# Performance work log

Hardware: AMD Instinct MI355X
Metric: run time of the kernel (lower is better)

The kernel has to match this reference:

```python
import jax, jax.numpy as jnp
import numpy as np

B, C, H, W = 32, 512, 64, 64
K = 512  # num_embeddings == embedding_dim == C (required by the original view())
COMMIT = 0.25


def setup_inputs() -> dict:
    key = jax.random.key(0)
    k1, k2 = jax.random.split(key)
    x = jax.random.normal(k1, (B, C, H, W), dtype=jnp.float32)
    # nn.Embedding weight init: uniform(-1/K, 1/K)
    embed = jax.random.uniform(k2, (K, C), dtype=jnp.float32, minval=-1.0 / K, maxval=1.0 / K)
    return {"x": x, "embed": embed}


def reference(x, embed):
    # BCHW -> BHWC
    inputs = jnp.transpose(x, (0, 2, 3, 1))  # [B,H,W,C]
    flat = inputs.reshape(-1, C)              # [N,C], N = B*H*W
    d = (jnp.sum(flat * flat, axis=1, keepdims=True)
         + jnp.sum(embed * embed, axis=1)
         - 2.0 * flat @ embed.T)              # [N,K]
    idx = jnp.argmin(d, axis=1)               # [N]
    # one-hot @ embed  ==  gather
    quantized = embed[idx].reshape(inputs.shape)  # [B,H,W,C]

    e_latent = jnp.mean((jax.lax.stop_gradient(quantized) - inputs) ** 2)
    q_latent = jnp.mean((quantized - jax.lax.stop_gradient(inputs)) ** 2)
    loss = q_latent + COMMIT * e_latent

    # straight-through estimator
    quant_st = inputs + jax.lax.stop_gradient(quantized - inputs)

    # perplexity (as in source: mean over batch of #unique codes used)
    idx_b = idx.reshape(B, -1)                # [B, H*W]

    def n_unique(i):
        cnt = jnp.zeros((K,), jnp.int32).at[i].add(1)
        return jnp.sum(cnt > 0)

    perplexity = jnp.mean(jax.vmap(n_unique)(idx_b).astype(jnp.float32))

    return loss, jnp.transpose(quant_st, (0, 3, 1, 2)), perplexity, idx_b
```

## Files before the change

kernel.cpp:

```cpp
#include <hip/hip_runtime.h>
#include <stdint.h>

#define B_ 32
#define C_ 512
#define HW_ 4096
#define N_ 131072
#define K_ 512
#define QELEMS 67108864
#define MARGIN 1e-3f
#define CAND   2.5e-3f
#define MAXC   16
#define RFCAP 131072

typedef __attribute__((ext_vector_type(8)))  short bf16x8;
typedef __attribute__((ext_vector_type(16))) float f32x16;

__device__ __forceinline__ ushort f2bf(float f) {
  uint u = __float_as_uint(f);
  return (ushort)((u + 0x7FFFu + ((u >> 16) & 1u)) >> 16);
}

__device__ __forceinline__ float np_pw512(const float* a) {
  float P[4];
#pragma unroll
  for (int m = 0; m < 4; ++m) {
    const float* q = a + m * 128;
    float rv[16];
#pragma unroll
    for (int l = 0; l < 16; ++l) {
      float v0 = q[l],      v1 = q[16 + l],  v2 = q[32 + l],  v3 = q[48 + l];
      float v4 = q[64 + l], v5 = q[80 + l],  v6 = q[96 + l],  v7 = q[112 + l];
      rv[l] = ((v0 + v1) + (v2 + v3)) + ((v4 + v5) + (v6 + v7));
    }
    float u[8], w[4];
#pragma unroll
    for (int l = 0; l < 8; ++l) u[l] = rv[8 + l] + rv[l];
#pragma unroll
    for (int l = 0; l < 4; ++l) w[l] = u[4 + l] + u[l];
    P[m] = (w[0] + w[2]) + (w[1] + w[3]);
  }
  return (P[0] + P[1]) + (P[2] + P[3]);
}

__device__ __forceinline__ float np_pw512_sq(const float* a) {
  float P[4];
#pragma unroll
  for (int m = 0; m < 4; ++m) {
    const float* q = a + m * 128;
    float rv[16];
#pragma unroll
    for (int l = 0; l < 16; ++l) {
      float v0 = __fmul_rn(q[l], q[l]);
      float v1 = __fmul_rn(q[16 + l], q[16 + l]);
      float v2 = __fmul_rn(q[32 + l], q[32 + l]);
      float v3 = __fmul_rn(q[48 + l], q[48 + l]);
      float v4 = __fmul_rn(q[64 + l], q[64 + l]);
      float v5 = __fmul_rn(q[80 + l], q[80 + l]);
      float v6 = __fmul_rn(q[96 + l], q[96 + l]);
      float v7 = __fmul_rn(q[112 + l], q[112 + l]);
      rv[l] = ((v0 + v1) + (v2 + v3)) + ((v4 + v5) + (v6 + v7));
    }
    float u[8], w[4];
#pragma unroll
    for (int l = 0; l < 8; ++l) u[l] = rv[8 + l] + rv[l];
#pragma unroll
    for (int l = 0; l < 4; ++l) w[l] = u[4 + l] + u[l];
    P[m] = (w[0] + w[2]) + (w[1] + w[3]);
  }
  return (P[0] + P[1]) + (P[2] + P[3]);
}

__global__ __launch_bounds__(256) void k_prep(const float* __restrict__ embed,
    float* __restrict__ senp, float* __restrict__ eT, int* __restrict__ rcnt,
    int* __restrict__ ocnt, int* __restrict__ candCnt)
{
  __shared__ float sqa[C_];
  int k = blockIdx.x;
  candCnt[blockIdx.x * 256 + threadIdx.x] = 0;
  for (int c = threadIdx.x; c < C_; c += 256) {
    float e = embed[k * C_ + c];
    eT[c * K_ + k] = e;
    sqa[c] = __fmul_rn(e, e);
  }
  __syncthreads();
  if (threadIdx.x == 0) {
    senp[k] = np_pw512(sqa);
    if (blockIdx.x == 0) { *rcnt = 0; *ocnt = 0; }
  }
}

__global__ __launch_bounds__(256) void k_epack(const float* __restrict__ embed,
    ushort* __restrict__ efrag)
{
  const int cb = blockIdx.x;
  const int t = threadIdx.x;
  const int lane = t & 63, ksq = t >> 6;
  const int l31 = lane & 31, lhi = lane >> 5;
  const float* ep = embed + ((size_t)(cb * 32 + l31) << 9) + lhi * 8;
#pragma unroll
  for (int i = 0; i < 8; ++i) {
    int ks = ksq * 8 + i;
    float4 v0 = *(const float4*)(ep + ks * 16);
    float4 v1 = *(const float4*)(ep + ks * 16 + 4);
    uint u0 = (uint)f2bf(v0.x) | ((uint)f2bf(v0.y) << 16);
    uint u1 = (uint)f2bf(v0.z) | ((uint)f2bf(v0.w) << 16);
    uint u2 = (uint)f2bf(v1.x) | ((uint)f2bf(v1.y) << 16);
    uint u3 = (uint)f2bf(v1.z) | ((uint)f2bf(v1.w) << 16);
    ushort* op = efrag + (((size_t)(cb * 32 + ks)) * 64 + lane) * 8;
    *(uint4*)op = make_uint4(u0, u1, u2, u3);
  }
}

__global__ __launch_bounds__(256) void k_xsplit(const float* __restrict__ x,
    ushort* __restrict__ xfrag, float* __restrict__ xT)
{
  __shared__ float tile[64][66];
  const int bid = blockIdx.x;
  const int ht = bid & 63, ct = (bid >> 6) & 7, b = bid >> 9;
  const int t = threadIdx.x;
  const int r = t & 63, cq = t >> 6;
  const float* xp = x + (((size_t)(b * C_ + ct * 64)) << 12) + ht * 64 + r;
#pragma unroll
  for (int i = 0; i < 16; ++i) {
    int c = cq * 16 + i;
    tile[r][c] = xp[(size_t)c << 12];
  }
  __syncthreads();
  const int lane = t & 63, ksl = t >> 6;
  const int l31 = lane & 31, lhi = lane >> 5;
  const int ks = ct * 4 + ksl;
  const int cc = ksl * 16 + lhi * 8;
#pragma unroll
  for (int rbl = 0; rbl < 2; ++rbl) {
    int rr = rbl * 32 + l31;
    uint u[4];
#pragma unroll
    for (int j = 0; j < 4; ++j) {
      float f0 = tile[rr][cc + 2 * j];
      float f1 = tile[rr][cc + 2 * j + 1];
      u[j] = (uint)f2bf(f0) | ((uint)f2bf(f1) << 16);
    }
    size_t rb = (size_t)b * 128 + ht * 2 + rbl;
    ushort* op = xfrag + ((rb * 32 + ks) * 64 + lane) * 8;
    *(uint4*)op = make_uint4(u[0], u[1], u[2], u[3]);
  }
  if (xT) {
    const int r2 = t >> 2, cs2 = (t & 3) << 4;
    float* op = xT + ((size_t)(b * HW_ + ht * 64 + r2) << 9) + ct * 64 + cs2;
#pragma unroll
    for (int j = 0; j < 4; ++j) {
      float4 v;
      v.x = tile[r2][cs2 + 4 * j + 0];
      v.y = tile[r2][cs2 + 4 * j + 1];
      v.z = tile[r2][cs2 + 4 * j + 2];
      v.w = tile[r2][cs2 + 4 * j + 3];
      *(float4*)(op + 4 * j) = v;
    }
  }
}

__global__ __launch_bounds__(512, 2) void k_argmin(const ushort* __restrict__ xfrag,
    const ushort* __restrict__ efrag, const float* __restrict__ senp,
    int* __restrict__ idx_out, int* __restrict__ rcnt, int* __restrict__ rrows,
    int* __restrict__ candCnt, int* __restrict__ cand)
{
  __shared__ float ses[K_];
  __shared__ float mbL[128][4], msL[128][4];
  __shared__ int   miL[128][4];
  __shared__ float rowBest[128];
  __shared__ int   rowFlag[128];
  const int t = threadIdx.x;
  const int lane = t & 63, wid = t >> 6;
  const int wc = wid & 3, wr = wid >> 2;
  const int l31 = lane & 31, lhi = lane >> 5;
  const int bid = blockIdx.x;

  for (int i = t; i < K_; i += 512) ses[i] = senp[i];
  __syncthreads();

  const size_t rb0 = (size_t)bid * 4 + wr * 2;
  const bf16x8* xq0 = (const bf16x8*)xfrag + rb0 * 2048 + lane;
  const bf16x8* xq1 = xq0 + 2048;
  const bf16x8* eq0 = (const bf16x8*)efrag + (size_t)(wc * 4 + 0) * 2048 + lane;
  const bf16x8* eq1 = eq0 + 2048;
  const bf16x8* eq2 = eq0 + 4096;
  const bf16x8* eq3 = eq0 + 6144;

  f32x16 z = {0,0,0,0,0,0,0,0,0,0,0,0,0,0,0,0};
  f32x16 a00 = z, a01 = z, a02 = z, a03 = z;
  f32x16 a10 = z, a11 = z, a12 = z, a13 = z;
  __builtin_amdgcn_s_setprio(1);
#pragma unroll 8
  for (int ks = 0; ks < 32; ++ks) {
    bf16x8 x0 = xq0[ks * 64];
    bf16x8 x1 = xq1[ks * 64];
    bf16x8 e0 = eq0[ks * 64];
    bf16x8 e1 = eq1[ks * 64];
    bf16x8 e2 = eq2[ks * 64];
    bf16x8 e3 = eq3[ks * 64];
    a00 = __builtin_amdgcn_mfma_f32_32x32x16_bf16(e0, x0, a00, 0, 0, 0);
    a01 = __builtin_amdgcn_mfma_f32_32x32x16_bf16(e1, x0, a01, 0, 0, 0);
    a02 = __builtin_amdgcn_mfma_f32_32x32x16_bf16(e2, x0, a02, 0, 0, 0);
    a03 = __builtin_amdgcn_mfma_f32_32x32x16_bf16(e3, x0, a03, 0, 0, 0);
    a10 = __builtin_amdgcn_mfma_f32_32x32x16_bf16(e0, x1, a10, 0, 0, 0);
    a11 = __builtin_amdgcn_mfma_f32_32x32x16_bf16(e1, x1, a11, 0, 0, 0);
    a12 = __builtin_amdgcn_mfma_f32_32x32x16_bf16(e2, x1, a12, 0, 0, 0);
    a13 = __builtin_amdgcn_mfma_f32_32x32x16_bf16(e3, x1, a13, 0, 0, 0);
  }
  __builtin_amdgcn_s_setprio(0);

  float b0 = 1e30f, s0 = 1e30f; int i0 = 0;
#pragma unroll
  for (int r = 0; r < 16; ++r) {
    int crow = (r & 3) + 8 * (r >> 2) + 4 * lhi;
    float v; int code;
    code = wc * 128 + 0  + crow; v = ses[code] - 2.0f * a00[r];
    if (v < b0 || (v == b0 && code < i0)) { s0 = b0; b0 = v; i0 = code; }
    else if (v < s0) s0 = v;
    code = wc * 128 + 32 + crow; v = ses[code] - 2.0f * a01[r];
    if (v < b0 || (v == b0 && code < i0)) { s0 = b0; b0 = v; i0 = code; }
    else if (v < s0) s0 = v;
    code = wc * 128 + 64 + crow; v = ses[code] - 2.0f * a02[r];
    if (v < b0 || (v == b0 && code < i0)) { s0 = b0; b0 = v; i0 = code; }
    else if (v < s0) s0 = v;
    code = wc * 128 + 96 + crow; v = ses[code] - 2.0f * a03[r];
    if (v < b0 || (v == b0 && code < i0)) { s0 = b0; b0 = v; i0 = code; }
    else if (v < s0) s0 = v;
  }
  float b1 = 1e30f, s1 = 1e30f; int i1 = 0;
#pragma unroll
  for (int r = 0; r < 16; ++r) {
    int crow = (r & 3) + 8 * (r >> 2) + 4 * lhi;
    float v; int code;
    code = wc * 128 + 0  + crow; v = ses[code] - 2.0f * a10[r];
    if (v < b1 || (v == b1 && code < i1)) { s1 = b1; b1 = v; i1 = code; }
    else if (v < s1) s1 = v;
    code = wc * 128 + 32 + crow; v = ses[code] - 2.0f * a11[r];
    if (v < b1 || (v == b1 && code < i1)) { s1 = b1; b1 = v; i1 = code; }
    else if (v < s1) s1 = v;
    code = wc * 128 + 64 + crow; v = ses[code] - 2.0f * a12[r];
    if (v < b1 || (v == b1 && code < i1)) { s1 = b1; b1 = v; i1 = code; }
    else if (v < s1) s1 = v;
    code = wc * 128 + 96 + crow; v = ses[code] - 2.0f * a13[r];
    if (v < b1 || (v == b1 && code < i1)) { s1 = b1; b1 = v; i1 = code; }
    else if (v < s1) s1 = v;
  }
  const float pb0 = b0, ps0 = s0; const int pi0 = i0;
  const float pb1 = b1, ps1 = s1; const int pi1 = i1;
  {
    float ob = __shfl_xor(b0, 32, 64), os = __shfl_xor(s0, 32, 64);
    int   oi = __shfl_xor(i0, 32, 64);
    float ns = fminf(fmaxf(b0, ob), fminf(s0, os));
    if (ob < b0 || (ob == b0 && oi < i0)) { b0 = ob; i0 = oi; }
    s0 = ns;
  }
  {
    float ob = __shfl_xor(b1, 32, 64), os = __shfl_xor(s1, 32, 64);
    int   oi = __shfl_xor(i1, 32, 64);
    float ns = fminf(fmaxf(b1, ob), fminf(s1, os));
    if (ob < b1 || (ob == b1 && oi < i1)) { b1 = ob; i1 = oi; }
    s1 = ns;
  }
  if (lane < 32) {
    int rr0 = (wr * 2 + 0) * 32 + l31;
    int rr1 = (wr * 2 + 1) * 32 + l31;
    mbL[rr0][wc] = b0; msL[rr0][wc] = s0; miL[rr0][wc] = i0;
    mbL[rr1][wc] = b1; msL[rr1][wc] = s1; miL[rr1][wc] = i1;
  }
  __syncthreads();
  if (t < 128) {
    float Bv = 1e30f, Sv = 1e30f; int Iv = 0;
#pragma unroll
    for (int q = 0; q < 4; ++q) {
      float bq = mbL[t][q], sq = msL[t][q]; int iq = miL[t][q];
      if (bq < Bv || (bq == Bv && iq < Iv)) { Sv = fminf(Bv, sq); Bv = bq; Iv = iq; }
      else Sv = fminf(Sv, bq);
    }
    int n = bid * 128 + t;
    idx_out[n] = Iv;
    rowBest[t] = Bv;
    int fl = (Sv - Bv < MARGIN) ? 1 : 0;
    rowFlag[t] = fl;
    if (fl) {
      int p = atomicAdd(rcnt, 1);
      if (p < RFCAP) rrows[p] = n;
    }
  }
  __syncthreads();
  {
    const int rr0 = (wr * 2 + 0) * 32 + l31;
    if (rowFlag[rr0]) {
      const float thr = rowBest[rr0] + CAND;
      const int n = bid * 128 + rr0;
      if (pb0 <= thr) {
        int p = atomicAdd(&candCnt[n], 1);
        if (p < MAXC) cand[(size_t)n * MAXC + p] = pi0;
      }
      if (ps0 <= thr) {
#pragma unroll
        for (int r = 0; r < 16; ++r) {
          int crow = (r & 3) + 8 * (r >> 2) + 4 * lhi;
          float v; int code;
          code = wc * 128 + 0  + crow; v = ses[code] - 2.0f * a00[r];
          if (v <= thr && code != pi0) { int p = atomicAdd(&candCnt[n], 1); if (p < MAXC) cand[(size_t)n * MAXC + p] = code; }
          code = wc * 128 + 32 + crow; v = ses[code] - 2.0f * a01[r];
          if (v <= thr && code != pi0) { int p = atomicAdd(&candCnt[n], 1); if (p < MAXC) cand[(size_t)n * MAXC + p] = code; }
          code = wc * 128 + 64 + crow; v = ses[code] - 2.0f * a02[r];
          if (v <= thr && code != pi0) { int p = atomicAdd(&candCnt[n], 1); if (p < MAXC) cand[(size_t)n * MAXC + p] = code; }
          code = wc * 128 + 96 + crow; v = ses[code] - 2.0f * a03[r];
          if (v <= thr && code != pi0) { int p = atomicAdd(&candCnt[n], 1); if (p < MAXC) cand[(size_t)n * MAXC + p] = code; }
        }
      }
    }
    const int rr1 = (wr * 2 + 1) * 32 + l31;
    if (rowFlag[rr1]) {
      const float thr = rowBest[rr1] + CAND;
      const int n = bid * 128 + rr1;
      if (pb1 <= thr) {
        int p = atomicAdd(&candCnt[n], 1);
        if (p < MAXC) cand[(size_t)n * MAXC + p] = pi1;
      }
      if (ps1 <= thr) {
#pragma unroll
        for (int r = 0; r < 16; ++r) {
          int crow = (r & 3) + 8 * (r >> 2) + 4 * lhi;
          float v; int code;
          code = wc * 128 + 0  + crow; v = ses[code] - 2.0f * a10[r];
          if (v <= thr && code != pi1) { int p = atomicAdd(&candCnt[n], 1); if (p < MAXC) cand[(size_t)n * MAXC + p] = code; }
          code = wc * 128 + 32 + crow; v = ses[code] - 2.0f * a11[r];
          if (v <= thr && code != pi1) { int p = atomicAdd(&candCnt[n], 1); if (p < MAXC) cand[(size_t)n * MAXC + p] = code; }
          code = wc * 128 + 64 + crow; v = ses[code] - 2.0f * a12[r];
          if (v <= thr && code != pi1) { int p = atomicAdd(&candCnt[n], 1); if (p < MAXC) cand[(size_t)n * MAXC + p] = code; }
          code = wc * 128 + 96 + crow; v = ses[code] - 2.0f * a13[r];
          if (v <= thr && code != pi1) { int p = atomicAdd(&candCnt[n], 1); if (p < MAXC) cand[(size_t)n * MAXC + p] = code; }
        }
      }
    }
  }
}

__global__ __launch_bounds__(256) void k_refine(const float* __restrict__ x,
    const float* __restrict__ xT, const float* __restrict__ embed,
    const float* __restrict__ senp,
    const int* __restrict__ rcnt, const int* __restrict__ rrows,
    const int* __restrict__ candCnt, const int* __restrict__ cand,
    int* __restrict__ ocnt, int* __restrict__ olist,
    int* __restrict__ idx_out)
{
  __shared__ float xls[4][516];
  __shared__ float SxSh[4];
  __shared__ int   nrow[4];
  const int t = threadIdx.x;
  const int lane = t & 63, w = t >> 6;
  int cnt = *rcnt; if (cnt > RFCAP) cnt = RFCAP;
  for (int base = blockIdx.x * 4; base < cnt; base += gridDim.x * 4) {
    __syncthreads();
    if (t < 4) {
      int i = base + t;
      nrow[t] = rrows[i < cnt ? i : base];
    }
    __syncthreads();
    if (xT) {
      for (int i = t; i < 4 * C_; i += 256) {
        int s = i >> 9, c = i & 511;
        xls[s][c] = xT[((size_t)nrow[s] << 9) + c];
      }
    } else {
      for (int i = t; i < 4 * C_; i += 256) {
        int s = i >> 9, c = i & 511;
        int n = nrow[s];
        int b = n >> 12, hw = n & 4095;
        xls[s][c] = x[(((size_t)(b * C_ + c)) << 12) + hw];
      }
    }
    __syncthreads();
    if (t < 4) SxSh[t] = np_pw512_sq(&xls[t][0]);
    __syncthreads();
    const int n = nrow[w];
    const int cc = candCnt[n];
    float d = 1e30f; int code = 0x7fffffff;
    if (cc <= MAXC) {
      if (lane < cc) {
        code = cand[(size_t)n * MAXC + lane];
        const float* e = embed + (size_t)code * C_;
        const float* xr = &xls[w][0];
        float s1 = 0.f, s2 = 0.f;
        for (int c = 0; c < 384; ++c)  s1 = fmaf(xr[c], e[c], s1);
        for (int c = 384; c < 512; ++c) s2 = fmaf(xr[c], e[c], s2);
        float M = s1 + s2;
        d = (SxSh[w] + senp[code]) - 2.0f * M;
      }
#pragma unroll
      for (int off = 1; off < 16; off <<= 1) {
        float ov = __shfl_xor(d, off, 64);
        int   oc = __shfl_xor(code, off, 64);
        if (ov < d || (ov == d && oc < code)) { d = ov; code = oc; }
      }
      if (lane == 0 && base + w < cnt) idx_out[n] = code;
    } else {
      if (lane == 0 && base + w < cnt) {
        int p = atomicAdd(ocnt, 1);
        if (p < RFCAP) olist[p] = n;
      }
    }
  }
}

__global__ __launch_bounds__(512) void k_refine_full(const float* __restrict__ x,
    const float* __restrict__ xT, const float* __restrict__ eT,
    const float* __restrict__ senp,
    const int* __restrict__ rcnt, const int* __restrict__ rrows,
    int* __restrict__ idx_out)
{
  __shared__ float xls[8][520];
  __shared__ float SxSh[8];
  __shared__ int   nrow[8];
  __shared__ float wval[8][8];
  __shared__ int   widx[8][8];
  const int t = threadIdx.x;
  const int lane = t & 63, w = t >> 6;
  int cnt = *rcnt; if (cnt > RFCAP) cnt = RFCAP;
  for (int base = blockIdx.x * 8; base < cnt; base += gridDim.x * 8) {
    __syncthreads();
    if (t < 8) {
      int i = base + t;
      nrow[t] = rrows[i < cnt ? i : base];
    }
    __syncthreads();
    if (xT) {
#pragma unroll
      for (int rr = 0; rr < 8; ++rr)
        xls[rr][t] = xT[((size_t)nrow[rr] << 9) + t];
    } else {
#pragma unroll
      for (int rr = 0; rr < 8; ++rr) {
        int n = nrow[rr];
        int b = n >> 12, hw = n & 4095;
        xls[rr][t] = x[(((size_t)(b * C_ + t)) << 12) + hw];
      }
    }
    __syncthreads();
    if (t < 8) SxSh[t] = np_pw512_sq(&xls[t][0]);
    __syncthreads();
    const float* ep = eT + t;
    float a1[8], a2[8];
#pragma unroll
    for (int rr = 0; rr < 8; ++rr) { a1[rr] = 0.f; a2[rr] = 0.f; }
    for (int c4 = 0; c4 < 384; c4 += 4) {
      float e0 = ep[(size_t)(c4 + 0) << 9];
      float e1 = ep[(size_t)(c4 + 1) << 9];
      float e2 = ep[(size_t)(c4 + 2) << 9];
      float e3 = ep[(size_t)(c4 + 3) << 9];
#pragma unroll
      for (int rr = 0; rr < 8; ++rr) {
        float4 xv = *(const float4*)&xls[rr][c4];
        a1[rr] = fmaf(xv.x, e0, a1[rr]);
        a1[rr] = fmaf(xv.y, e1, a1[rr]);
        a1[rr] = fmaf(xv.z, e2, a1[rr]);
        a1[rr] = fmaf(xv.w, e3, a1[rr]);
      }
    }
    for (int c4 = 384; c4 < 512; c4 += 4) {
      float e0 = ep[(size_t)(c4 + 0) << 9];
      float e1 = ep[(size_t)(c4 + 1) << 9];
      float e2 = ep[(size_t)(c4 + 2) << 9];
      float e3 = ep[(size_t)(c4 + 3) << 9];
#pragma unroll
      for (int rr = 0; rr < 8; ++rr) {
        float4 xv = *(const float4*)&xls[rr][c4];
        a2[rr] = fmaf(xv.x, e0, a2[rr]);
        a2[rr] = fmaf(xv.y, e1, a2[rr]);
        a2[rr] = fmaf(xv.z, e2, a2[rr]);
        a2[rr] = fmaf(xv.w, e3, a2[rr]);
      }
    }
    float se = senp[t];
    float bv[8]; int bi[8];
#pragma unroll
    for (int rr = 0; rr < 8; ++rr) {
      float M = a1[rr] + a2[rr];
      bv[rr] = (SxSh[rr] + se) - 2.0f * M;
      bi[rr] = t;
    }
#pragma unroll
    for (int off = 1; off < 64; off <<= 1) {
#pragma unroll
      for (int rr = 0; rr < 8; ++rr) {
        float ov = __shfl_xor(bv[rr], off, 64);
        int   oi = __shfl_xor(bi[rr], off, 64);
        if (ov < bv[rr] || (ov == bv[rr] && oi < bi[rr])) { bv[rr] = ov; bi[rr] = oi; }
      }
    }
    if (lane == 0) {
#pragma unroll
      for (int rr = 0; rr < 8; ++rr) { wval[w][rr] = bv[rr]; widx[w][rr] = bi[rr]; }
    }
    __syncthreads();
    if (t < 8) {
      float Bv = wval[0][t]; int Iv = widx[0][t];
#pragma unroll
      for (int q = 1; q < 8; ++q) {
        float ov = wval[q][t]; int oi = widx[q][t];
        if (ov < Bv || (ov == Bv && oi < Iv)) { Bv = ov; Iv = oi; }
      }
      if (base + t < cnt) idx_out[nrow[t]] = Iv;
    }
  }
}

__global__ __launch_bounds__(256) void k_gather(const float* __restrict__ x,
    const float* __restrict__ embed, const int* __restrict__ idx,
    float* __restrict__ out_q, double* __restrict__ loss_part)
{
  __shared__ float ecol[32][512];
  const int bid = blockIdx.x;
  const int hch = bid & 1, cch = (bid >> 1) & 15, b = bid >> 5;
  const int c0 = cch * 32, hw0 = hch * 2048;
  const int t = threadIdx.x;
  for (int i = t; i < 512 * 32; i += 256) {
    int c = i & 31, k = i >> 5;
    ecol[c][(k + c0 + c) & 511] = embed[((size_t)k << 9) + c0 + c];
  }
  __syncthreads();
  int kreg[8];
#pragma unroll
  for (int j = 0; j < 8; ++j)
    kreg[j] = idx[(b << 12) + hw0 + t + 256 * j];
  double s = 0.0;
  for (int c = 0; c < 32; ++c) {
    const float* xrow = x + (((size_t)(b * C_ + c0 + c)) << 12) + hw0;
    float* orow = out_q + (((size_t)(b * C_ + c0 + c)) << 12) + hw0;
#pragma unroll
    for (int j = 0; j < 8; ++j) {
      float q  = ecol[c][(kreg[j] + c0 + c) & 511];
      float xv = xrow[t + 256 * j];
      orow[t + 256 * j] = q;
      double d = (double)q - (double)xv;
      s += d * d;
    }
  }
  for (int off = 32; off > 0; off >>= 1) s += __shfl_down(s, off, 64);
  __shared__ double wsum[4];
  if ((t & 63) == 0) wsum[t >> 6] = s;
  __syncthreads();
  if (t == 0)
    loss_part[bid] = (wsum[0] + wsum[1]) + (wsum[2] + wsum[3]);
}

__global__ __launch_bounds__(256) void k_pplx(const int* __restrict__ idx,
    float* __restrict__ out_idxf, int* __restrict__ counts)
{
  __shared__ int flags[K_];
  __shared__ int red[256];
  int b = blockIdx.x;
  for (int i = threadIdx.x; i < K_; i += 256) flags[i] = 0;
  __syncthreads();
  for (int hw = threadIdx.x; hw < HW_; hw += 256) {
    int k = idx[(b << 12) + hw];
    flags[k] = 1;
    out_idxf[(b << 12) + hw] = (float)k;
  }
  __syncthreads();
  int c = 0;
  for (int i = threadIdx.x; i < K_; i += 256) c += flags[i];
  red[threadIdx.x] = c;
  __syncthreads();
  for (int st = 128; st > 0; st >>= 1) {
    if (threadIdx.x < st) red[threadIdx.x] += red[threadIdx.x + st];
    __syncthreads();
  }
  if (threadIdx.x == 0) counts[b] = red[0];
}

__global__ __launch_bounds__(256) void k_final(const double* __restrict__ loss_part,
    const int* __restrict__ counts, float* __restrict__ out_loss,
    float* __restrict__ out_pplx)
{
  __shared__ double sred[256];
  double s = 0.0;
  for (int i = threadIdx.x; i < 1024; i += 256) s += loss_part[i];
  sred[threadIdx.x] = s;
  __syncthreads();
  for (int st = 128; st > 0; st >>= 1) {
    if (threadIdx.x < st) sred[threadIdx.x] += sred[threadIdx.x + st];
    __syncthreads();
  }
  if (threadIdx.x == 0) {
    *out_loss = (float)(1.25 * sred[0] / (double)QELEMS);
    int c = 0;
    for (int i = 0; i < B_; ++i) c += counts[i];
    *out_pplx = (float)c / (float)B_;
  }
}

extern "C" void kernel_launch(void* const* d_in, const int* in_sizes, int n_in,
                              void* d_out, int out_size, void* d_ws, size_t ws_size,
                              hipStream_t stream)
{
  const float* x     = (const float*)d_in[0];
  const float* embed = (const float*)d_in[1];
  float* out      = (float*)d_out;
  float* out_loss = out;
  float* out_q    = out + 1;
  float* out_pplx = out + 1 + QELEMS;
  float* out_idxf = out + 2 + QELEMS;

  char* ws = (char*)d_ws;
  int*    w_idx = (int*)ws;
  double* w_lp  = (double*)(ws + 524288);
  int*    w_cnt = (int*)(ws + 524288 + 16384);
  size_t pers = 524288 + 16384 + 128;

  const size_t SZ_XFR  = 134217728;
  const size_t SZ_EFR  = 524288;
  const size_t SZ_SENP = 2048;
  const size_t SZ_RCNT = 256;
  const size_t SZ_RROW = (size_t)RFCAP * 4;
  const size_t SZ_OLST = (size_t)RFCAP * 4;
  const size_t SZ_ET   = (size_t)K_ * C_ * 4;
  const size_t SZ_CCNT = (size_t)N_ * 4;
  const size_t SZ_CAND = (size_t)N_ * MAXC * 4;
  const size_t SZ_XT   = (size_t)N_ * C_ * 4;
  const size_t VOL_SMALL = SZ_XFR + SZ_EFR + SZ_SENP + SZ_RCNT + SZ_RROW +
                           SZ_OLST + SZ_ET + SZ_CCNT + SZ_CAND;
  const size_t VOL_BIG   = VOL_SMALL + SZ_XT;

  char* vbase;
  float* w_xT = nullptr;
  if (ws_size >= pers + VOL_BIG + 4096) {
    vbase = ws + ((pers + 255) & ~(size_t)255);
    w_xT  = (float*)(vbase + VOL_SMALL);
  } else if (ws_size >= pers + VOL_SMALL + 4096) {
    vbase = ws + ((pers + 255) & ~(size_t)255);
  } else {
    uintptr_t a = ((uintptr_t)(out_q + QELEMS) - VOL_SMALL) & ~(uintptr_t)255;
    vbase = (char*)a;
  }
  char* p = vbase;
  ushort* w_xfr  = (ushort*)p;            p += SZ_XFR;
  ushort* w_efr  = (ushort*)p;            p += SZ_EFR;
  float*  w_senp = (float*)p;             p += SZ_SENP;
  int*    w_rcnt = (int*)p;
  int*    w_ocnt = (int*)(p + 128);       p += SZ_RCNT;
  int*    w_rrows= (int*)p;               p += SZ_RROW;
  int*    w_olst = (int*)p;               p += SZ_OLST;
  float*  w_eT   = (float*)p;             p += SZ_ET;
  int*    w_ccnt = (int*)p;               p += SZ_CCNT;
  int*    w_cand = (int*)p;               p += SZ_CAND;

  k_prep  <<<dim3(512),   dim3(256), 0, stream>>>(embed, w_senp, w_eT, w_rcnt, w_ocnt, w_ccnt);
  k_epack <<<dim3(16),    dim3(256), 0, stream>>>(embed, w_efr);
  k_xsplit<<<dim3(16384), dim3(256), 0, stream>>>(x, w_xfr, w_xT);
  k_argmin<<<dim3(1024),  dim3(512), 0, stream>>>(w_xfr, w_efr, w_senp, w_idx, w_rcnt, w_rrows, w_ccnt, w_cand);
  k_refine<<<dim3(2048),  dim3(256), 0, stream>>>(x, w_xT, embed, w_senp, w_rcnt, w_rrows, w_ccnt, w_cand, w_ocnt, w_olst, w_idx);
  k_refine_full<<<dim3(256), dim3(512), 0, stream>>>(x, w_xT, w_eT, w_senp, w_ocnt, w_olst, w_idx);
  k_gather<<<dim3(1024),  dim3(256), 0, stream>>>(x, embed, w_idx, out_q, w_lp);
  k_pplx  <<<dim3(32),    dim3(256), 0, stream>>>(w_idx, out_idxf, w_cnt);
  k_final <<<dim3(1),     dim3(256), 0, stream>>>(w_lp, w_cnt, out_loss, out_pplx);
}
```

Measured before the change: 532.0 us.

## Stage argmin GEMM operands through double-buffered LDS via direct global-to-LDS loads

The argmin kernel no longer has each wave load its own x and codebook fragments straight from global memory. The block now cooperatively loads each k-slice of x and all codebook fragments into a double-buffered shared-memory stage using global_load_lds, prefetching the next slice while the MFMAs run on the current one. This removes the redundant global/L2 reads of the codebook across waves and overlaps memory with compute. In exchange it adds a block-wide barrier every k-step, uses about 40KB more LDS (which may limit the two-blocks-per-CU occupancy), and removes the unroll pragma.

```diff
diff --git a/kernel.cpp b/kernel.cpp
--- a/kernel.cpp
+++ b/kernel.cpp
@@ -169,6 +169,7 @@
   __shared__ int   miL[128][4];
   __shared__ float rowBest[128];
   __shared__ int   rowFlag[128];
+  __shared__ __align__(16) ushort stg[2 * 20 * 512];
   const int t = threadIdx.x;
   const int lane = t & 63, wid = t >> 6;
   const int wc = wid & 3, wr = wid >> 2;
@@ -176,28 +177,45 @@
   const int bid = blockIdx.x;
 
   for (int i = t; i < K_; i += 512) ses[i] = senp[i];
-  __syncthreads();
-
-  const size_t rb0 = (size_t)bid * 4 + wr * 2;
-  const bf16x8* xq0 = (const bf16x8*)xfrag + rb0 * 2048 + lane;
-  const bf16x8* xq1 = xq0 + 2048;
-  const bf16x8* eq0 = (const bf16x8*)efrag + (size_t)(wc * 4 + 0) * 2048 + lane;
-  const bf16x8* eq1 = eq0 + 2048;
-  const bf16x8* eq2 = eq0 + 4096;
-  const bf16x8* eq3 = eq0 + 6144;
+
+  const ushort* g0 = (wid < 4)
+      ? xfrag + ((size_t)(bid * 4 + wid) * 2048 + lane) * 8
+      : efrag + ((size_t)(wid - 4) * 2048 + lane) * 8;
+  const ushort* g1 = efrag + ((size_t)(wid + 4) * 2048 + lane) * 8;
+  const ushort* g2 = efrag + ((size_t)(wid + 12) * 2048 + lane) * 8;
+
+  auto GLL = [&](const ushort* gp, int lofs) {
+    __builtin_amdgcn_global_load_lds(
+        (const __attribute__((address_space(1))) uint32_t*)gp,
+        (__attribute__((address_space(3))) uint32_t*)&stg[lofs], 16, 0, 0);
+  };
+
+  GLL(g0, wid * 512);
+  GLL(g1, (wid + 8) * 512);
+  if (wid < 4) GLL(g2, (wid + 16) * 512);
+  __syncthreads();
 
   f32x16 z = {0,0,0,0,0,0,0,0,0,0,0,0,0,0,0,0};
   f32x16 a00 = z, a01 = z, a02 = z, a03 = z;
   f32x16 a10 = z, a11 = z, a12 = z, a13 = z;
-  __builtin_amdgcn_s_setprio(1);
-#pragma unroll 8
+
   for (int ks = 0; ks < 32; ++ks) {
-    bf16x8 x0 = xq0[ks * 64];
-    bf16x8 x1 = xq1[ks * 64];
-    bf16x8 e0 = eq0[ks * 64];
-    bf16x8 e1 = eq1[ks * 64];
-    bf16x8 e2 = eq2[ks * 64];
-    bf16x8 e3 = eq3[ks * 64];
+    const int cur = ks & 1;
+    if (ks + 1 < 32) {
+      const size_t so = (size_t)(ks + 1) * 512;
+      const int bo = (cur ^ 1) * (20 * 512);
+      GLL(g0 + so, bo + wid * 512);
+      GLL(g1 + so, bo + (wid + 8) * 512);
+      if (wid < 4) GLL(g2 + so, bo + (wid + 16) * 512);
+    }
+    const ushort* bp = &stg[cur * (20 * 512)];
+    bf16x8 x0 = *(const bf16x8*)(bp + (wr * 2 + 0) * 512 + lane * 8);
+    bf16x8 x1 = *(const bf16x8*)(bp + (wr * 2 + 1) * 512 + lane * 8);
+    bf16x8 e0 = *(const bf16x8*)(bp + (4 + wc * 4 + 0) * 512 + lane * 8);
+    bf16x8 e1 = *(const bf16x8*)(bp + (4 + wc * 4 + 1) * 512 + lane * 8);
+    bf16x8 e2 = *(const bf16x8*)(bp + (4 + wc * 4 + 2) * 512 + lane * 8);
+    bf16x8 e3 = *(const bf16x8*)(bp + (4 + wc * 4 + 3) * 512 + lane * 8);
+    __builtin_amdgcn_s_setprio(1);
     a00 = __builtin_amdgcn_mfma_f32_32x32x16_bf16(e0, x0, a00, 0, 0, 0);
     a01 = __builtin_amdgcn_mfma_f32_32x32x16_bf16(e1, x0, a01, 0, 0, 0);
     a02 = __builtin_amdgcn_mfma_f32_32x32x16_bf16(e2, x0, a02, 0, 0, 0);
@@ -206,8 +224,9 @@
     a11 = __builtin_amdgcn_mfma_f32_32x32x16_bf16(e1, x1, a11, 0, 0, 0);
     a12 = __builtin_amdgcn_mfma_f32_32x32x16_bf16(e2, x1, a12, 0, 0, 0);
     a13 = __builtin_amdgcn_mfma_f32_32x32x16_bf16(e3, x1, a13, 0, 0, 0);
-  }
-  __builtin_amdgcn_s_setprio(0);
+    __builtin_amdgcn_s_setprio(0);
+    __syncthreads();
+  }
 
   float b0 = 1e30f, s0 = 1e30f; int i0 = 0;
 #pragma unroll
```

Result: no change. 523.9 us (median of 2 runs) (-1.5%).
